# Kernel tuning notes

Hardware: AMD Instinct MI355X
Metric: run time of the kernel (lower is better)

## Reference

```python
import jax, jax.numpy as jnp
import numpy as np

# dims
B, S, H, D = 1, 2048, 32, 128
BLOCK = 64          # sparse_block_size
LOCAL = 16          # local_blocks
VERT = 8            # vert_stride
OFFSET = 0          # head_sliding_offset
SLIDE = max(1, VERT // H)  # head_sliding_step = max(1, int(vert_stride / num_heads))
NEG_INF = -1e30


def _sparse_mask():
    """Token-level local+vertical-stride causal mask, [H, S, S] bool."""
    pos = jnp.arange(S)
    blk = pos // BLOCK                                  # block index per token
    causal = pos[:, None] >= pos[None, :]               # [S, S]
    local = (blk[:, None] - blk[None, :]) < LOCAL       # [S, S]
    h = jnp.arange(H)
    # per-head vertical strips on key blocks
    vert = ((blk[None, None, :] + h[:, None, None] * SLIDE + OFFSET + 1) % VERT) == 0  # [H,1,S]
    return causal[None, :, :] & (local[None, :, :] | vert)  # [H, S, S]


def setup_inputs() -> dict:
    key = jax.random.key(0)
    kq, kk, kv = jax.random.split(key, 3)
    shape = (B, S, H, D)
    return {
        "query": jax.random.normal(kq, shape, dtype=jnp.float32),
        "key": jax.random.normal(kk, shape, dtype=jnp.float32),
        "value": jax.random.normal(kv, shape, dtype=jnp.float32),
    }


def reference(query, key, value):
    # inputs are bshd; sm_scale = head_dim**-0.5 (dkernel default)
    scale = 1.0 / jnp.sqrt(jnp.asarray(D, dtype=query.dtype))
    mask = _sparse_mask()                               # [H, S, S]
    scores = jnp.einsum("bqhd,bkhd->bhqk", query, key) * scale
    scores = jnp.where(mask[None], scores, NEG_INF)
    probs = jax.nn.softmax(scores, axis=-1)
    out = jnp.einsum("bhqk,bkhd->bqhd", probs, value)
    return out
```

## Files before the change

kernel.cpp:

```cpp
#include <hip/hip_runtime.h>


#define NH 32
#define HD 128
#define LOCALB 16

typedef __attribute__((ext_vector_type(8))) short short8;
typedef __attribute__((ext_vector_type(4))) float f32x4;

static __device__ __forceinline__ unsigned f2u(float f) {
    union { float f; unsigned u; } x; x.f = f; return x.u;
}
static __device__ __forceinline__ unsigned bfpk(float a, float b) {
    return ((f2u(a) + 0x8000u) >> 16) | ((f2u(b) + 0x8000u) & 0xFFFF0000u);
}
static __device__ __forceinline__ unsigned short f2bf(float f) {
    return (unsigned short)((f2u(f) + 0x8000u) >> 16);
}

static __device__ __forceinline__ void wg_barrier() {
    asm volatile("" ::: "memory");
    __builtin_amdgcn_s_waitcnt(0xC07F);
    __builtin_amdgcn_s_barrier();
    asm volatile("" ::: "memory");
}

static __device__ __forceinline__ bool blk_active(int qb, int kb, int h) {
    return ((qb - kb) < LOCALB) || (((kb + h + 1) & 7) == 0);
}

static __device__ __forceinline__ int krow(int kk) {
    return (kk & 3) | (((kk >> 2) & 1) << 4) | (((kk >> 3) & 3) << 2) | (kk & 32);
}

__global__ __launch_bounds__(256)
void prepack_kv(const float* __restrict__ K, const float* __restrict__ V,
                char* __restrict__ W)
{
    const int id  = blockIdx.x;
    const int kb  = id >> 5;
    const int h   = id & 31;
    const int tid = threadIdx.x;
    char* tile = W + ((size_t)((h << 5) | kb) << 15);

    __shared__ __align__(16) float Vf[64][128];

    {
        const float* vsrc = V + (size_t)kb * 262144 + h * 128;
        #pragma unroll
        for (int it = 0; it < 8; ++it) {
            const int f  = it * 1024 + tid * 4;
            const int ky = f >> 7;
            const int d0 = f & 127;
            const float4 v = *reinterpret_cast<const float4*>(vsrc + (size_t)ky * 4096 + d0);
            const int dd = d0 ^ (((ky >> 3) & 7) << 2);
            *reinterpret_cast<float4*>(&Vf[ky][dd]) = v;
        }
    }

    #pragma unroll
    for (int it = 0; it < 4; ++it) {
        const int o    = tid * 16 + it * 4096;
        const int nt   = o >> 12;
        const int ks   = (o >> 10) & 3;
        const int quad = (o >> 8) & 3;
        const int m16  = (o >> 4) & 15;
        const int row  = nt * 16 + m16;
        const int kk   = (row & 3) | (((row >> 4) & 1) << 2)
                       | (((row >> 2) & 3) << 3) | (row & 32);
        const float* src = K + (size_t)(kb * 64 + kk) * 4096 + h * 128
                             + ks * 32 + quad * 8;
        const float4 a = *reinterpret_cast<const float4*>(src);
        const float4 b = *reinterpret_cast<const float4*>(src + 4);
        uint4 pk;
        pk.x = bfpk(a.x, a.y); pk.y = bfpk(a.z, a.w);
        pk.z = bfpk(b.x, b.y); pk.w = bfpk(b.z, b.w);
        *reinterpret_cast<uint4*>(tile + o) = pk;
    }

    __syncthreads();

    #pragma unroll
    for (int it = 0; it < 4; ++it) {
        const int o    = tid * 16 + it * 4096;
        const int dt   = o >> 11;
        const int c    = (o >> 10) & 1;
        const int quad = (o >> 8) & 3;
        const int m16  = (o >> 4) & 15;
        const int d    = dt * 16 + m16;
        const int g    = c * 4 + quad;
        const int dd   = d ^ (g << 2);
        const float x0 = Vf[8 * g + 0][dd], x1 = Vf[8 * g + 1][dd];
        const float x2 = Vf[8 * g + 2][dd], x3 = Vf[8 * g + 3][dd];
        const float x4 = Vf[8 * g + 4][dd], x5 = Vf[8 * g + 5][dd];
        const float x6 = Vf[8 * g + 6][dd], x7 = Vf[8 * g + 7][dd];
        uint4 pk;
        pk.x = bfpk(x0, x1); pk.y = bfpk(x2, x3);
        pk.z = bfpk(x4, x5); pk.w = bfpk(x6, x7);
        *reinterpret_cast<uint4*>(tile + 16384 + o) = pk;
    }
}

__global__ __launch_bounds__(256) __attribute__((amdgpu_waves_per_eu(2, 2)))
void sparse_attn_fast(const float* __restrict__ Q,
                      const char* __restrict__ W,
                      float* __restrict__ O)
{
    const int id   = blockIdx.x;
    const int h    = (id & 7) * 4 + ((id >> 3) & 3);
    const int qb   = 31 - (id >> 5);

    const int tid  = threadIdx.x;
    const int wave = tid >> 6;
    const int lane = tid & 63;
    const int m16  = lane & 15;
    const int quad = lane >> 4;
    const int lb   = lane << 4;

    const float QSC = 0.08838834764831845f * 1.44269504088896f;
    short8 qf[4];
    {
        const int qrow = qb * 64 + wave * 16 + m16;
        const float* qp = Q + ((size_t)qrow * NH + h) * HD + quad * 8;
        #pragma unroll
        for (int ks = 0; ks < 4; ++ks) {
            const float4 a = *reinterpret_cast<const float4*>(qp + ks * 32);
            const float4 b = *reinterpret_cast<const float4*>(qp + ks * 32 + 4);
            short8 f;
            f[0]=(short)f2bf(a.x*QSC); f[1]=(short)f2bf(a.y*QSC);
            f[2]=(short)f2bf(a.z*QSC); f[3]=(short)f2bf(a.w*QSC);
            f[4]=(short)f2bf(b.x*QSC); f[5]=(short)f2bf(b.y*QSC);
            f[6]=(short)f2bf(b.z*QSC); f[7]=(short)f2bf(b.w*QSC);
            qf[ks] = f;
        }
    }

    f32x4 acc[8];
    #pragma unroll
    for (int dt = 0; dt < 8; ++dt) { acc[dt][0]=0.f; acc[dt][1]=0.f; acc[dt][2]=0.f; acc[dt][3]=0.f; }
    float ls0 = 0.f, ls1 = 0.f;

    int kb = 0;
    while (!blk_active(qb, kb, h)) ++kb;
    int kh = 0;
    const char* tb = W + ((size_t)((h << 5) | kb) << 15);

    float4 kfA[8], vfA[8], kfB[8], vfB[8];

    #define LOAD32(KF, VF, TB, KH)                                              \
        { _Pragma("unroll")                                                     \
          for (int nt2 = 0; nt2 < 2; ++nt2) {                                   \
              _Pragma("unroll")                                                 \
              for (int ks = 0; ks < 4; ++ks)                                    \
                  KF[nt2 * 4 + ks] = *reinterpret_cast<const float4*>(          \
                      (TB) + (KH) * 8192 + nt2 * 4096 + ks * 1024 + lb);        \
          }                                                                     \
          _Pragma("unroll")                                                     \
          for (int dt = 0; dt < 8; ++dt)                                        \
              VF[dt] = *reinterpret_cast<const float4*>(                        \
                  (TB) + 16384 + dt * 2048 + (KH) * 1024 + lb); }

    #define BODY(KF, VF, NKF, NVF)                                              \
        {                                                                       \
            int nkb, nkh;                                                       \
            if (kh == 0) { nkb = kb; nkh = 1; }                                 \
            else {                                                              \
                nkb = kb + 1;                                                   \
                while (nkb <= qb && !blk_active(qb, nkb, h)) ++nkb;             \
                nkh = 0;                                                        \
            }                                                                   \
            const char* tbn = W + ((size_t)((h << 5) | (nkb & 31)) << 15);      \
            if (nkb <= qb) { LOAD32(NKF, NVF, tbn, nkh) }                       \
                                        \
            f32x4 sc0 = {0.f, 0.f, 0.f, 0.f};                                   \
            f32x4 sc1 = {0.f, 0.f, 0.f, 0.f};                                   \
            _Pragma("unroll")                                                   \
            for (int ks = 0; ks < 4; ++ks) {                                    \
                sc0 = __builtin_amdgcn_mfma_f32_16x16x32_bf16(                  \
                    *reinterpret_cast<const short8*>(&KF[ks]),     qf[ks], sc0, 0, 0, 0); \
                sc1 = __builtin_amdgcn_mfma_f32_16x16x32_bf16(                  \
                    *reinterpret_cast<const short8*>(&KF[4 + ks]), qf[ks], sc1, 0, 0, 0); \
            }                                                                   \
                    \
            if (kb == qb) {                                                     \
                const int qloc = wave * 16 + m16;                               \
                const int k0 = kh * 32 + quad * 8;                              \
                _Pragma("unroll")                                               \
                for (int r = 0; r < 4; ++r) {                                   \
                    if (k0 + r > qloc)     sc0[r] = -1.0e30f;                   \
                    if (k0 + 4 + r > qloc) sc1[r] = -1.0e30f;                   \
                }                                                               \
            }                                                                   \
                                                       \
            _Pragma("unroll")                                                   \
            for (int r = 0; r < 4; ++r) {                                       \
                sc0[r] = __builtin_exp2f(sc0[r]);                               \
                sc1[r] = __builtin_exp2f(sc1[r]);                               \
            }                                                                   \
            ls0 += (sc0[0] + sc0[1]) + (sc0[2] + sc0[3]);                       \
            ls1 += (sc1[0] + sc1[1]) + (sc1[2] + sc1[3]);                       \
                                           \
            union { unsigned u[4]; short8 s; } cv;                              \
            cv.u[0] = bfpk(sc0[0], sc0[1]);                                     \
            cv.u[1] = bfpk(sc0[2], sc0[3]);                                     \
            cv.u[2] = bfpk(sc1[0], sc1[1]);                                     \
            cv.u[3] = bfpk(sc1[2], sc1[3]);                                     \
            const short8 pf = cv.s;                                             \
                                                            \
            _Pragma("unroll")                                                   \
            for (int dt = 0; dt < 8; ++dt)                                      \
                acc[dt] = __builtin_amdgcn_mfma_f32_16x16x32_bf16(              \
                    *reinterpret_cast<const short8*>(&VF[dt]), pf, acc[dt], 0, 0, 0); \
            kb = nkb; kh = nkh; tb = tbn;                                       \
        }

    LOAD32(kfA, vfA, tb, 0)

    while (true) {
        BODY(kfA, vfA, kfB, vfB)
        if (kb > qb) break;
        BODY(kfB, vfB, kfA, vfA)
        if (kb > qb) break;
    }

    #undef BODY
    #undef LOAD32

    float l = ls0 + ls1;
    l += __shfl_xor(l, 16);
    l += __shfl_xor(l, 32);
    const float inv = 1.0f / l;

    float* op = O + ((size_t)(qb * 64 + wave * 16 + m16) * NH + h) * HD + quad * 4;
    #pragma unroll
    for (int dt = 0; dt < 8; ++dt) {
        f32x4 v = acc[dt];
        v[0] *= inv; v[1] *= inv; v[2] *= inv; v[3] *= inv;
        *reinterpret_cast<f32x4*>(op + dt * 16) = v;
    }
}

__global__ __launch_bounds__(256)
void sparse_attn_kernel(const float* __restrict__ Q,
                        const float* __restrict__ K,
                        const float* __restrict__ V,
                        float* __restrict__ O)
{
    const int id   = blockIdx.x;
    const int h    = (id & 7) * 4 + ((id >> 3) & 3);
    const int qb   = 31 - (id >> 5);

    const int tid  = threadIdx.x;
    const int wave = tid >> 6;
    const int lane = tid & 63;
    const int m16  = lane & 15;
    const int quad = lane >> 4;

    __shared__ __align__(16) char smem[64 * 136 * 2 + 128 * 36 * 4];
    unsigned short (*Ks)[136] = reinterpret_cast<unsigned short(*)[136]>(smem);
    unsigned (*Vp)[36] = reinterpret_cast<unsigned(*)[36]>(smem + 64 * 136 * 2);

    const float QSC = 0.08838834764831845f * 1.44269504088896f;
    short8 qf[4];
    {
        const int qrow = qb * 64 + wave * 16 + m16;
        const float* qp = Q + ((size_t)qrow * NH + h) * HD + quad * 8;
        #pragma unroll
        for (int ks = 0; ks < 4; ++ks) {
            const float4 a = *reinterpret_cast<const float4*>(qp + ks * 32);
            const float4 b = *reinterpret_cast<const float4*>(qp + ks * 32 + 4);
            short8 f;
            f[0]=(short)f2bf(a.x*QSC); f[1]=(short)f2bf(a.y*QSC);
            f[2]=(short)f2bf(a.z*QSC); f[3]=(short)f2bf(a.w*QSC);
            f[4]=(short)f2bf(b.x*QSC); f[5]=(short)f2bf(b.y*QSC);
            f[6]=(short)f2bf(b.z*QSC); f[7]=(short)f2bf(b.w*QSC);
            qf[ks] = f;
        }
    }

    f32x4 acc[8];
    #pragma unroll
    for (int dt = 0; dt < 8; ++dt) { acc[dt][0]=0.f; acc[dt][1]=0.f; acc[dt][2]=0.f; acc[dt][3]=0.f; }
    float mrow = -3.0e38f;
    float lrow = 0.f;

    const int kkey0 = tid >> 5;
    const int kd4   = (tid & 31) << 2;
    const int vkey0 = wave * 8 + (lane & 7);
    const int vd40  = (lane >> 3) << 2;
    const int vc    = wave * 4 + ((lane & 7) >> 1);

    int kb = 0;
    while (!blk_active(qb, kb, h)) ++kb;

    float4 kreg[8], vreg[8];
    {
        const float* kp = K + (size_t)kb * 262144 + (size_t)kkey0 * 4096 + h * 128 + kd4;
        #pragma unroll
        for (int it = 0; it < 8; ++it)
            kreg[it] = *reinterpret_cast<const float4*>(kp + it * 32768);
        const float* vp = V + (size_t)kb * 262144 + (size_t)vkey0 * 4096 + h * 128 + vd40;
        #pragma unroll
        for (int it = 0; it < 8; ++it)
            vreg[it] = *reinterpret_cast<const float4*>(vp + (it & 1) * 131072 + (it >> 1) * 32);
    }

    while (kb <= qb) {
        int nkb = kb + 1;
        while (nkb <= qb && !blk_active(qb, nkb, h)) ++nkb;

        wg_barrier();

        #pragma unroll
        for (int it = 0; it < 8; ++it) {
            const float4 kv = kreg[it];
            uint2 pk; pk.x = bfpk(kv.x, kv.y); pk.y = bfpk(kv.z, kv.w);
            *reinterpret_cast<uint2*>(&Ks[krow(it * 8 + kkey0)][kd4]) = pk;
        }
        if (nkb <= qb) {
            const float* kp = K + (size_t)nkb * 262144 + (size_t)kkey0 * 4096 + h * 128 + kd4;
            #pragma unroll
            for (int it = 0; it < 8; ++it)
                kreg[it] = *reinterpret_cast<const float4*>(kp + it * 32768);
        }

        #pragma unroll
        for (int it = 0; it < 8; ++it) {
            const int d4 = (it >> 1) * 32 + vd40;
            const float4 vv = vreg[it];
            const unsigned p0 = bfpk(vv.x, vv.y);
            const unsigned p1 = bfpk(vv.z, vv.w);
            const unsigned q0 = __shfl_xor(p0, 1);
            const unsigned q1 = __shfl_xor(p1, 1);
            const int c = (it & 1) * 16 + vc;
            if ((lane & 1) == 0) {
                Vp[d4 + 0][c] = (p0 & 0xFFFFu) | (q0 << 16);
                Vp[d4 + 1][c] = (p0 >> 16)     | (q0 & 0xFFFF0000u);
            } else {
                Vp[d4 + 2][c] = (q1 & 0xFFFFu) | (p1 << 16);
                Vp[d4 + 3][c] = (q1 >> 16)     | (p1 & 0xFFFF0000u);
            }
        }
        if (nkb <= qb) {
            const float* vp = V + (size_t)nkb * 262144 + (size_t)vkey0 * 4096 + h * 128 + vd40;
            #pragma unroll
            for (int it = 0; it < 8; ++it)
                vreg[it] = *reinterpret_cast<const float4*>(vp + (it & 1) * 131072 + (it >> 1) * 32);
        }

        wg_barrier();

        f32x4 sc[4];
        #pragma unroll
        for (int nt = 0; nt < 4; ++nt) {
            f32x4 s = {0.f, 0.f, 0.f, 0.f};
            #pragma unroll
            for (int ks = 0; ks < 4; ++ks) {
                const short8 a = *reinterpret_cast<const short8*>(&Ks[nt * 16 + m16][ks * 32 + quad * 8]);
                s = __builtin_amdgcn_mfma_f32_16x16x32_bf16(a, qf[ks], s, 0, 0, 0);
            }
            sc[nt] = s;
        }

        if (kb == qb) {
            const int qloc = wave * 16 + m16;
            #pragma unroll
            for (int nt = 0; nt < 4; ++nt) {
                const int kb0 = (nt >> 1) * 32 + quad * 8 + (nt & 1) * 4;
                #pragma unroll
                for (int r = 0; r < 4; ++r) {
                    if (kb0 + r > qloc) sc[nt][r] = -1.0e30f;
                }
            }
        }

        float mx = sc[0][0];
        #pragma unroll
        for (int nt = 0; nt < 4; ++nt) {
            #pragma unroll
            for (int r = 0; r < 4; ++r) mx = fmaxf(mx, sc[nt][r]);
        }
        mx = fmaxf(mx, __shfl_xor(mx, 16));
        mx = fmaxf(mx, __shfl_xor(mx, 32));
        const float mnew = fmaxf(mrow, mx);
        const float alpha = __builtin_exp2f(mrow - mnew);
        lrow *= alpha;
        #pragma unroll
        for (int dt = 0; dt < 8; ++dt) {
            acc[dt][0] *= alpha; acc[dt][1] *= alpha;
            acc[dt][2] *= alpha; acc[dt][3] *= alpha;
        }
        float rs = 0.f;
        #pragma unroll
        for (int nt = 0; nt < 4; ++nt) {
            #pragma unroll
            for (int r = 0; r < 4; ++r) {
                const float p = __builtin_exp2f(sc[nt][r] - mnew);
                sc[nt][r] = p;
                rs += p;
            }
        }
        rs += __shfl_xor(rs, 16);
        rs += __shfl_xor(rs, 32);
        lrow += rs;
        mrow = mnew;

        short8 pf[2];
        #pragma unroll
        for (int c = 0; c < 2; ++c) {
            union { unsigned u[4]; short8 s; } cv;
            cv.u[0] = bfpk(sc[2 * c][0],     sc[2 * c][1]);
            cv.u[1] = bfpk(sc[2 * c][2],     sc[2 * c][3]);
            cv.u[2] = bfpk(sc[2 * c + 1][0], sc[2 * c + 1][1]);
            cv.u[3] = bfpk(sc[2 * c + 1][2], sc[2 * c + 1][3]);
            pf[c] = cv.s;
        }

        #pragma unroll
        for (int dt = 0; dt < 8; ++dt) {
            #pragma unroll
            for (int c = 0; c < 2; ++c) {
                const short8 a = *reinterpret_cast<const short8*>(
                    &Vp[dt * 16 + m16][c * 16 + quad * 4]);
                acc[dt] = __builtin_amdgcn_mfma_f32_16x16x32_bf16(a, pf[c], acc[dt], 0, 0, 0);
            }
        }

        kb = nkb;
    }

    __syncthreads();
    float* Osf = reinterpret_cast<float*>(smem);
    {
        const float inv = 1.0f / lrow;
        const int q = wave * 16 + m16;
        #pragma unroll
        for (int dt = 0; dt < 8; ++dt) {
            f32x4 v = acc[dt];
            v[0] *= inv; v[1] *= inv; v[2] *= inv; v[3] *= inv;
            *reinterpret_cast<f32x4*>(&Osf[q * 132 + dt * 16 + quad * 4]) = v;
        }
    }
    __syncthreads();
    #pragma unroll
    for (int p = 0; p < 2; ++p) {
        const int row = p * 32 + (tid >> 3);
        const int dbase = (tid & 7) * 4;
        #pragma unroll
        for (int i = 0; i < 4; ++i) {
            const int d = i * 32 + dbase;
            const f32x4 v = *reinterpret_cast<const f32x4*>(&Osf[row * 132 + d]);
            *reinterpret_cast<f32x4*>(O + ((size_t)(qb * 64 + row) * NH + h) * HD + d) = v;
        }
    }
}

extern "C" void kernel_launch(void* const* d_in, const int* in_sizes, int n_in,
                              void* d_out, int out_size, void* d_ws, size_t ws_size,
                              hipStream_t stream) {
    const float* q = (const float*)d_in[0];
    const float* k = (const float*)d_in[1];
    const float* v = (const float*)d_in[2];
    float* out = (float*)d_out;
    if (d_ws != nullptr && ws_size >= (size_t)33554432) {
        prepack_kv<<<dim3(1024), dim3(256), 0, stream>>>(k, v, (char*)d_ws);
        sparse_attn_fast<<<dim3(1024), dim3(256), 0, stream>>>(q, (const char*)d_ws, out);
    } else {
        sparse_attn_kernel<<<dim3(1024), dim3(256), 0, stream>>>(q, k, v, out);
    }
}
```

Measured before the change: 187.7 us.

## Process two adjacent query blocks per workgroup to reuse K/V tiles

New measurement: 183.3 us. 2.3% less time.

```diff
diff --git a/kernel.cpp b/kernel.cpp
--- a/kernel.cpp
+++ b/kernel.cpp
@@ -108,7 +108,9 @@
 {
     const int id   = blockIdx.x;
     const int h    = (id & 7) * 4 + ((id >> 3) & 3);
-    const int qb   = 31 - (id >> 5);
+    const int pr   = id >> 5;
+    const int qb1  = 31 - 2 * pr;
+    const int qb0  = qb1 - 1;
 
     const int tid  = threadIdx.x;
     const int wave = tid >> 6;
@@ -118,125 +120,156 @@
     const int lb   = lane << 4;
 
     const float QSC = 0.08838834764831845f * 1.44269504088896f;
-    short8 qf[4];
+    short8 qf0[4], qf1[4];
     {
-        const int qrow = qb * 64 + wave * 16 + m16;
-        const float* qp = Q + ((size_t)qrow * NH + h) * HD + quad * 8;
+        const int qr0 = qb0 * 64 + wave * 16 + m16;
+        const int qr1 = qb1 * 64 + wave * 16 + m16;
+        const float* qp0 = Q + ((size_t)qr0 * NH + h) * HD + quad * 8;
+        const float* qp1 = Q + ((size_t)qr1 * NH + h) * HD + quad * 8;
         #pragma unroll
         for (int ks = 0; ks < 4; ++ks) {
-            const float4 a = *reinterpret_cast<const float4*>(qp + ks * 32);
-            const float4 b = *reinterpret_cast<const float4*>(qp + ks * 32 + 4);
+            const float4 a0 = *reinterpret_cast<const float4*>(qp0 + ks * 32);
+            const float4 b0 = *reinterpret_cast<const float4*>(qp0 + ks * 32 + 4);
+            const float4 a1 = *reinterpret_cast<const float4*>(qp1 + ks * 32);
+            const float4 b1 = *reinterpret_cast<const float4*>(qp1 + ks * 32 + 4);
             short8 f;
-            f[0]=(short)f2bf(a.x*QSC); f[1]=(short)f2bf(a.y*QSC);
-            f[2]=(short)f2bf(a.z*QSC); f[3]=(short)f2bf(a.w*QSC);
-            f[4]=(short)f2bf(b.x*QSC); f[5]=(short)f2bf(b.y*QSC);
-            f[6]=(short)f2bf(b.z*QSC); f[7]=(short)f2bf(b.w*QSC);
-            qf[ks] = f;
-        }
-    }
-
-    f32x4 acc[8];
+            f[0]=(short)f2bf(a0.x*QSC); f[1]=(short)f2bf(a0.y*QSC);
+            f[2]=(short)f2bf(a0.z*QSC); f[3]=(short)f2bf(a0.w*QSC);
+            f[4]=(short)f2bf(b0.x*QSC); f[5]=(short)f2bf(b0.y*QSC);
+            f[6]=(short)f2bf(b0.z*QSC); f[7]=(short)f2bf(b0.w*QSC);
+            qf0[ks] = f;
+            short8 g;
+            g[0]=(short)f2bf(a1.x*QSC); g[1]=(short)f2bf(a1.y*QSC);
+            g[2]=(short)f2bf(a1.z*QSC); g[3]=(short)f2bf(a1.w*QSC);
+            g[4]=(short)f2bf(b1.x*QSC); g[5]=(short)f2bf(b1.y*QSC);
+            g[6]=(short)f2bf(b1.z*QSC); g[7]=(short)f2bf(b1.w*QSC);
+            qf1[ks] = g;
+        }
+    }
+
+    f32x4 acc0[8], acc1[8];
     #pragma unroll
-    for (int dt = 0; dt < 8; ++dt) { acc[dt][0]=0.f; acc[dt][1]=0.f; acc[dt][2]=0.f; acc[dt][3]=0.f; }
-    float ls0 = 0.f, ls1 = 0.f;
+    for (int dt = 0; dt < 8; ++dt) {
+        acc0[dt][0]=0.f; acc0[dt][1]=0.f; acc0[dt][2]=0.f; acc0[dt][3]=0.f;
+        acc1[dt][0]=0.f; acc1[dt][1]=0.f; acc1[dt][2]=0.f; acc1[dt][3]=0.f;
+    }
+    float la = 0.f, lb2 = 0.f;
 
     int kb = 0;
-    while (!blk_active(qb, kb, h)) ++kb;
+    while (!blk_active(qb0, kb, h)) ++kb;
     int kh = 0;
     const char* tb = W + ((size_t)((h << 5) | kb) << 15);
 
-    float4 kfA[8], vfA[8], kfB[8], vfB[8];
-
-    #define LOAD32(KF, VF, TB, KH)                                              \
+    float4 kfA[8], kfB[8];
+
+    #define LOADK(KF, TB, KH)                                                   \
         { _Pragma("unroll")                                                     \
           for (int nt2 = 0; nt2 < 2; ++nt2) {                                   \
               _Pragma("unroll")                                                 \
               for (int ks = 0; ks < 4; ++ks)                                    \
                   KF[nt2 * 4 + ks] = *reinterpret_cast<const float4*>(          \
                       (TB) + (KH) * 8192 + nt2 * 4096 + ks * 1024 + lb);        \
-          }                                                                     \
-          _Pragma("unroll")                                                     \
-          for (int dt = 0; dt < 8; ++dt)                                        \
-              VF[dt] = *reinterpret_cast<const float4*>(                        \
-                  (TB) + 16384 + dt * 2048 + (KH) * 1024 + lb); }
-
-    #define BODY(KF, VF, NKF, NVF)                                              \
+          } }
+
+    #define BODY(KF, NKF)                                                       \
         {                                                                       \
             int nkb, nkh;                                                       \
             if (kh == 0) { nkb = kb; nkh = 1; }                                 \
             else {                                                              \
                 nkb = kb + 1;                                                   \
-                while (nkb <= qb && !blk_active(qb, nkb, h)) ++nkb;             \
+                while (nkb <= qb1 && !blk_active(qb0, nkb, h)) ++nkb;           \
                 nkh = 0;                                                        \
             }                                                                   \
+                     \
+            float4 vf[8];                                                       \
+            _Pragma("unroll")                                                   \
+            for (int dt = 0; dt < 8; ++dt)                                      \
+                vf[dt] = *reinterpret_cast<const float4*>(                      \
+                    tb + 16384 + dt * 2048 + kh * 1024 + lb);                   \
             const char* tbn = W + ((size_t)((h << 5) | (nkb & 31)) << 15);      \
-            if (nkb <= qb) { LOAD32(NKF, NVF, tbn, nkh) }                       \
-                                        \
-            f32x4 sc0 = {0.f, 0.f, 0.f, 0.f};                                   \
-            f32x4 sc1 = {0.f, 0.f, 0.f, 0.f};                                   \
+            if (nkb <= qb1) { LOADK(NKF, tbn, nkh) }                            \
+                                  \
+            f32x4 sa0 = {0.f,0.f,0.f,0.f}, sa1 = {0.f,0.f,0.f,0.f};             \
+            f32x4 sb0 = {0.f,0.f,0.f,0.f}, sb1 = {0.f,0.f,0.f,0.f};             \
             _Pragma("unroll")                                                   \
             for (int ks = 0; ks < 4; ++ks) {                                    \
-                sc0 = __builtin_amdgcn_mfma_f32_16x16x32_bf16(                  \
-                    *reinterpret_cast<const short8*>(&KF[ks]),     qf[ks], sc0, 0, 0, 0); \
-                sc1 = __builtin_amdgcn_mfma_f32_16x16x32_bf16(                  \
-                    *reinterpret_cast<const short8*>(&KF[4 + ks]), qf[ks], sc1, 0, 0, 0); \
+                const short8 a0 = *reinterpret_cast<const short8*>(&KF[ks]);    \
+                const short8 a1 = *reinterpret_cast<const short8*>(&KF[4 + ks]);\
+                sa0 = __builtin_amdgcn_mfma_f32_16x16x32_bf16(a0, qf0[ks], sa0, 0, 0, 0); \
+                sa1 = __builtin_amdgcn_mfma_f32_16x16x32_bf16(a1, qf0[ks], sa1, 0, 0, 0); \
+                sb0 = __builtin_amdgcn_mfma_f32_16x16x32_bf16(a0, qf1[ks], sb0, 0, 0, 0); \
+                sb1 = __builtin_amdgcn_mfma_f32_16x16x32_bf16(a1, qf1[ks], sb1, 0, 0, 0); \
             }                                                                   \
-                    \
-            if (kb == qb) {                                                     \
-                const int qloc = wave * 16 + m16;                               \
-                const int k0 = kh * 32 + quad * 8;                              \
-                _Pragma("unroll")                                               \
-                for (int r = 0; r < 4; ++r) {                                   \
-                    if (k0 + r > qloc)     sc0[r] = -1.0e30f;                   \
-                    if (k0 + 4 + r > qloc) sc1[r] = -1.0e30f;                   \
-                }                                                               \
+                          \
+            const bool vert = (((kb + h + 1) & 7) == 0);                        \
+            const bool act0 = (kb <= qb0) && (((qb0 - kb) < LOCALB) || vert);   \
+            const bool act1 = ((qb1 - kb) < LOCALB) || vert;                    \
+            const int qloc = wave * 16 + m16;                                   \
+            const int k0 = kh * 32 + quad * 8;                                  \
+            _Pragma("unroll")                                                   \
+            for (int r = 0; r < 4; ++r) {                                       \
+                if (!act0 || (kb == qb0 && k0 + r > qloc))     sa0[r] = -1.0e30f; \
+                if (!act0 || (kb == qb0 && k0 + 4 + r > qloc)) sa1[r] = -1.0e30f; \
+                if (!act1 || (kb == qb1 && k0 + r > qloc))     sb0[r] = -1.0e30f; \
+                if (!act1 || (kb == qb1 && k0 + 4 + r > qloc)) sb1[r] = -1.0e30f; \
             }                                                                   \
                                                        \
             _Pragma("unroll")                                                   \
             for (int r = 0; r < 4; ++r) {                                       \
-                sc0[r] = __builtin_exp2f(sc0[r]);                               \
-                sc1[r] = __builtin_exp2f(sc1[r]);                               \
+                sa0[r] = __builtin_exp2f(sa0[r]); sa1[r] = __builtin_exp2f(sa1[r]); \
+                sb0[r] = __builtin_exp2f(sb0[r]); sb1[r] = __builtin_exp2f(sb1[r]); \
             }                                                                   \
-            ls0 += (sc0[0] + sc0[1]) + (sc0[2] + sc0[3]);                       \
-            ls1 += (sc1[0] + sc1[1]) + (sc1[2] + sc1[3]);                       \
-                                           \
-            union { unsigned u[4]; short8 s; } cv;                              \
-            cv.u[0] = bfpk(sc0[0], sc0[1]);                                     \
-            cv.u[1] = bfpk(sc0[2], sc0[3]);                                     \
-            cv.u[2] = bfpk(sc1[0], sc1[1]);                                     \
-            cv.u[3] = bfpk(sc1[2], sc1[3]);                                     \
-            const short8 pf = cv.s;                                             \
-                                                            \
+            la  += ((sa0[0]+sa0[1])+(sa0[2]+sa0[3])) + ((sa1[0]+sa1[1])+(sa1[2]+sa1[3])); \
+            lb2 += ((sb0[0]+sb0[1])+(sb0[2]+sb0[3])) + ((sb1[0]+sb1[1])+(sb1[2]+sb1[3])); \
+                                                               \
+            union { unsigned u[4]; short8 s; } cva, cvb;                        \
+            cva.u[0] = bfpk(sa0[0], sa0[1]); cva.u[1] = bfpk(sa0[2], sa0[3]);   \
+            cva.u[2] = bfpk(sa1[0], sa1[1]); cva.u[3] = bfpk(sa1[2], sa1[3]);   \
+            cvb.u[0] = bfpk(sb0[0], sb0[1]); cvb.u[1] = bfpk(sb0[2], sb0[3]);   \
+            cvb.u[2] = bfpk(sb1[0], sb1[1]); cvb.u[3] = bfpk(sb1[2], sb1[3]);   \
+            const short8 pfa = cva.s;                                           \
+            const short8 pfb = cvb.s;                                           \
+                                  \
             _Pragma("unroll")                                                   \
-            for (int dt = 0; dt < 8; ++dt)                                      \
-                acc[dt] = __builtin_amdgcn_mfma_f32_16x16x32_bf16(              \
-                    *reinterpret_cast<const short8*>(&VF[dt]), pf, acc[dt], 0, 0, 0); \
+            for (int dt = 0; dt < 8; ++dt) {                                    \
+                const short8 av = *reinterpret_cast<const short8*>(&vf[dt]);    \
+                acc0[dt] = __builtin_amdgcn_mfma_f32_16x16x32_bf16(av, pfa, acc0[dt], 0, 0, 0); \
+                acc1[dt] = __builtin_amdgcn_mfma_f32_16x16x32_bf16(av, pfb, acc1[dt], 0, 0, 0); \
+            }                                                                   \
             kb = nkb; kh = nkh; tb = tbn;                                       \
         }
 
-    LOAD32(kfA, vfA, tb, 0)
+    LOADK(kfA, tb, 0)
 
     while (true) {
-        BODY(kfA, vfA, kfB, vfB)
-        if (kb > qb) break;
-        BODY(kfB, vfB, kfA, vfA)
-        if (kb > qb) break;
+        BODY(kfA, kfB)
+        if (kb > qb1) break;
+        BODY(kfB, kfA)
+        if (kb > qb1) break;
     }
 
     #undef BODY
-    #undef LOAD32
-
-    float l = ls0 + ls1;
-    l += __shfl_xor(l, 16);
-    l += __shfl_xor(l, 32);
-    const float inv = 1.0f / l;
-
-    float* op = O + ((size_t)(qb * 64 + wave * 16 + m16) * NH + h) * HD + quad * 4;
+    #undef LOADK
+
+    float l0 = la;
+    l0 += __shfl_xor(l0, 16);
+    l0 += __shfl_xor(l0, 32);
+    const float inv0 = 1.0f / l0;
+    float l1 = lb2;
+    l1 += __shfl_xor(l1, 16);
+    l1 += __shfl_xor(l1, 32);
+    const float inv1 = 1.0f / l1;
+
+    float* op0 = O + ((size_t)(qb0 * 64 + wave * 16 + m16) * NH + h) * HD + quad * 4;
+    float* op1 = O + ((size_t)(qb1 * 64 + wave * 16 + m16) * NH + h) * HD + quad * 4;
     #pragma unroll
     for (int dt = 0; dt < 8; ++dt) {
-        f32x4 v = acc[dt];
-        v[0] *= inv; v[1] *= inv; v[2] *= inv; v[3] *= inv;
-        *reinterpret_cast<f32x4*>(op + dt * 16) = v;
+        f32x4 v0 = acc0[dt];
+        v0[0] *= inv0; v0[1] *= inv0; v0[2] *= inv0; v0[3] *= inv0;
+        *reinterpret_cast<f32x4*>(op0 + dt * 16) = v0;
+        f32x4 v1 = acc1[dt];
+        v1[0] *= inv1; v1[1] *= inv1; v1[2] *= inv1; v1[3] *= inv1;
+        *reinterpret_cast<f32x4*>(op1 + dt * 16) = v1;
     }
 }
 
@@ -464,7 +497,7 @@
     float* out = (float*)d_out;
     if (d_ws != nullptr && ws_size >= (size_t)33554432) {
         prepack_kv<<<dim3(1024), dim3(256), 0, stream>>>(k, v, (char*)d_ws);
-        sparse_attn_fast<<<dim3(1024), dim3(256), 0, stream>>>(q, (const char*)d_ws, out);
+        sparse_attn_fast<<<dim3(512), dim3(256), 0, stream>>>(q, (const char*)d_ws, out);
     } else {
         sparse_attn_kernel<<<dim3(1024), dim3(256), 0, stream>>>(q, k, v, out);
     }
```
